# Performance work log

Measured on AMD Instinct MI355X. Metric: run time of the kernel, lower is better.

Reference implementation:

```python
import jax, jax.numpy as jnp
import numpy as np

H = 1024   # hidden_size
NH = 16    # num heads
DH = H // NH
L = 2      # attention levels
E = 8      # experts
F = 4 * H  # expert FFN hidden
B = 2
S = 1024
EPS = 1e-5
TOPK = 2
STD = 0.02


def setup_inputs() -> dict:
    key = jax.random.key(0)
    ks = jax.random.split(key, 12)
    def n(k, shp):
        return jax.random.normal(k, shp, jnp.float32) * STD
    return {
        "hidden_states": jax.random.normal(ks[0], (B, S, H), jnp.float32),
        "attention_mask": jnp.ones((B, S), jnp.int32),
        "ln1_g": jnp.ones((H,), jnp.float32), "ln1_b": jnp.zeros((H,), jnp.float32),
        "ln2_g": jnp.ones((H,), jnp.float32), "ln2_b": jnp.zeros((H,), jnp.float32),
        "Wq": n(ks[1], (L, H, H)), "Wk": n(ks[2], (L, H, H)),
        "Wv": n(ks[3], (L, H, H)), "Wo": n(ks[4], (L, H, H)),
        "bq": jnp.zeros((L, H), jnp.float32), "bk": jnp.zeros((L, H), jnp.float32),
        "bv": jnp.zeros((L, H), jnp.float32), "bo": jnp.zeros((L, H), jnp.float32),
        "level_logits": n(ks[5], (L,)),
        "Wr": n(ks[6], (H, E)), "br": jnp.zeros((E,), jnp.float32),
        "W1": n(ks[7], (E, H, F)), "b1": jnp.zeros((E, F), jnp.float32),
        "W2": n(ks[8], (E, F, H)), "b2": jnp.zeros((E, H), jnp.float32),
    }


def _ln(x, g, b):
    m = x.mean(-1, keepdims=True)
    v = x.var(-1, keepdims=True)
    return (x - m) * jax.lax.rsqrt(v + EPS) * g + b


def _mla(x, mask_f, Wq, Wk, Wv, Wo, bq, bk, bv, bo, level_logits):
    # Multi-level attention: one MHA per level, softmax-combined over levels.
    b_, s_, _ = x.shape
    def proj(W, bias):
        y = jnp.einsum('bsh,lhd->lbsd', x, W) + bias[:, None, None, :]
        return y.reshape(L, b_, s_, NH, DH)
    q, k, v = proj(Wq, bq), proj(Wk, bk), proj(Wv, bv)
    scores = jnp.einsum('lbqnd,lbknd->lbnqk', q, k) / np.float32(np.sqrt(DH))
    bias = (1.0 - mask_f)[None, :, None, None, :] * jnp.float32(-1e9)  # key-side mask
    attn = jax.nn.softmax(scores + bias, axis=-1)
    ctx = jnp.einsum('lbnqk,lbknd->lbqnd', attn, v).reshape(L, b_, s_, H)
    out = jnp.einsum('lbsh,lhd->lbsd', ctx, Wo) + bo[:, None, None, :]
    w = jax.nn.softmax(level_logits)
    return jnp.einsum('l,lbsd->bsd', w, out)


def _moe(x, Wr, br, W1, b1, W2, b2):
    # Top-2 softmax router with renormalized gates; dense expert compute,
    # sparse combine (math-equivalent to dispatch/combine without dropping).
    logits = x @ Wr + br                                  # [B,S,E]
    probs = jax.nn.softmax(logits, axis=-1)
    topv, topi = jax.lax.top_k(probs, TOPK)               # [B,S,K]
    gates = topv / topv.sum(-1, keepdims=True)
    combine = jnp.sum(jax.nn.one_hot(topi, E, dtype=x.dtype) * gates[..., None], axis=-2)  # [B,S,E]
    h = jax.nn.gelu(jnp.einsum('bsh,ehf->besf', x, W1) + b1[None, :, None, :])
    y = jnp.einsum('besf,efh->besh', h, W2) + b2[None, :, None, :]
    return jnp.einsum('bse,besh->bsh', combine, y), logits


def reference(hidden_states, attention_mask, ln1_g, ln1_b, ln2_g, ln2_b,
              Wq, Wk, Wv, Wo, bq, bk, bv, bo, level_logits,
              Wr, br, W1, b1, W2, b2):
    mask_f = attention_mask.astype(jnp.float32)
    attn = _mla(_ln(hidden_states, ln1_g, ln1_b), mask_f,
                Wq, Wk, Wv, Wo, bq, bk, bv, bo, level_logits)
    x = hidden_states + attn                  # residual 1 (dropout in eval = identity)
    moe_out, _router_logits = _moe(_ln(x, ln2_g, ln2_b), Wr, br, W1, b1, W2, b2)
    return x + moe_out                        # residual 2
```

## Files before the change

### kernel.cpp

```cpp
#include <hip/hip_runtime.h>
#include <hip/hip_bf16.h>
#include <stdint.h>

#define Hn   1024
#define NHn  16
#define DHn  64
#define Ln   2
#define En   8
#define Fn   4096
#define Bn   2
#define Sn   1024
#define Tn   2048
#define An   4096
#define KSPLIT 4

typedef __bf16 bf16_t;
typedef __bf16 bf16x2 __attribute__((ext_vector_type(2)));
typedef __bf16 bf16x4 __attribute__((ext_vector_type(4)));
typedef __bf16 bf16x8 __attribute__((ext_vector_type(8)));
typedef float  f32x4  __attribute__((ext_vector_type(4)));

__device__ __forceinline__ f32x4 mfma16(bf16x8 a, bf16x8 b, f32x4 c){
  return __builtin_amdgcn_mfma_f32_16x16x32_bf16(a, b, c, 0, 0, 0);
}
__device__ __forceinline__ void gload16(const void* gsrc, void* ldst){
  __builtin_amdgcn_global_load_lds((const __attribute__((address_space(1))) void*)gsrc,
                                   (__attribute__((address_space(3))) void*)ldst, 16, 0, 0);
}
__device__ __forceinline__ float gelu_f(float x){
  float u = 0.7978845608028654f * (x + 0.044715f * x * x * x);
  return 0.5f * x * (1.0f + tanhf(u));
}

__global__ __launch_bounds__(256)
void tcvt_k(const float* __restrict__ src, bf16_t* __restrict__ dst, int R, int C){
  __shared__ float tile[64][68];
  size_t moff = (size_t)blockIdx.z * R * C;
  src += moff; dst += moff;
  int c0 = blockIdx.x * 64, r0 = blockIdx.y * 64;
  int tid = threadIdx.x;
  int tx = tid & 15, ty = tid >> 4;
  #pragma unroll
  for (int i = 0; i < 4; ++i){
    float4 v = *(const float4*)(src + (size_t)(r0 + ty + i*16) * C + c0 + tx*4);
    *(float4*)&tile[ty + i*16][tx*4] = v;
  }
  __syncthreads();
  int c = tid >> 2, rq = tid & 3;
  #pragma unroll
  for (int i = 0; i < 2; ++i){
    int rr = (rq + i*4) * 8;
    bf16x8 pk;
    #pragma unroll
    for (int j = 0; j < 8; ++j) pk[j] = (bf16_t)tile[rr + j][c];
    *(bf16x8*)(dst + (size_t)(c0 + c) * R + r0 + rr) = pk;
  }
}

__global__ __launch_bounds__(256)
void ln_k(const float* __restrict__ x, const float* __restrict__ gam,
          const float* __restrict__ bet, bf16_t* __restrict__ out){
  int row = blockIdx.x;
  const float4* xr = (const float4*)(x + (size_t)row * Hn);
  int t = threadIdx.x, lane = t & 63, w = t >> 6;
  float4 v = xr[t];
  float s  = v.x + v.y + v.z + v.w;
  float ss = v.x*v.x + v.y*v.y + v.z*v.z + v.w*v.w;
  #pragma unroll
  for (int mk = 1; mk < 64; mk <<= 1){ s += __shfl_xor(s, mk); ss += __shfl_xor(ss, mk); }
  __shared__ float r1[4], r2[4];
  if (lane == 0){ r1[w] = s; r2[w] = ss; }
  __syncthreads();
  float S1 = r1[0]+r1[1]+r1[2]+r1[3];
  float S2 = r2[0]+r2[1]+r2[2]+r2[3];
  float mean = S1 * (1.0f/Hn);
  float var  = S2 * (1.0f/Hn) - mean*mean;
  float rstd = rsqrtf(var + 1e-5f);
  int c = t * 4;
  bf16_t* o = out + (size_t)row * Hn + c;
  o[0] = (bf16_t)((v.x-mean)*rstd*gam[c+0] + bet[c+0]);
  o[1] = (bf16_t)((v.y-mean)*rstd*gam[c+1] + bet[c+1]);
  o[2] = (bf16_t)((v.z-mean)*rstd*gam[c+2] + bet[c+2]);
  o[3] = (bf16_t)((v.w-mean)*rstd*gam[c+3] + bet[c+3]);
}

__global__ __launch_bounds__(256)
void res_ln2_k(const float* __restrict__ x, const float* __restrict__ o0,
               const float* __restrict__ o1, const float* __restrict__ lvl,
               const float* __restrict__ gam, const float* __restrict__ bet,
               float* __restrict__ x2, bf16_t* __restrict__ xn2){
  int row = blockIdx.x, t = threadIdx.x, lane = t & 63, w = t >> 6;
  float l0 = lvl[0], l1 = lvl[1];
  float mx = fmaxf(l0, l1);
  float e0 = __expf(l0 - mx), e1 = __expf(l1 - mx);
  float inv = 1.f / (e0 + e1);
  float w0 = e0 * inv, w1 = e1 * inv;
  size_t base = (size_t)row * Hn;
  float4 xv = ((const float4*)(x  + base))[t];
  float4 a0 = ((const float4*)(o0 + base))[t];
  float4 a1 = ((const float4*)(o1 + base))[t];
  float4 v;
  v.x = xv.x + w0*a0.x + w1*a1.x;
  v.y = xv.y + w0*a0.y + w1*a1.y;
  v.z = xv.z + w0*a0.z + w1*a1.z;
  v.w = xv.w + w0*a0.w + w1*a1.w;
  ((float4*)(x2 + base))[t] = v;
  float s  = v.x + v.y + v.z + v.w;
  float ss = v.x*v.x + v.y*v.y + v.z*v.z + v.w*v.w;
  #pragma unroll
  for (int mk = 1; mk < 64; mk <<= 1){ s += __shfl_xor(s, mk); ss += __shfl_xor(ss, mk); }
  __shared__ float r1[4], r2[4];
  if (lane == 0){ r1[w] = s; r2[w] = ss; }
  __syncthreads();
  float S1 = r1[0]+r1[1]+r1[2]+r1[3];
  float S2 = r2[0]+r2[1]+r2[2]+r2[3];
  float mean = S1 * (1.0f/Hn);
  float var  = S2 * (1.0f/Hn) - mean*mean;
  float rstd = rsqrtf(var + 1e-5f);
  int c = t * 4;
  bf16_t* o = xn2 + base + c;
  o[0] = (bf16_t)((v.x-mean)*rstd*gam[c+0] + bet[c+0]);
  o[1] = (bf16_t)((v.y-mean)*rstd*gam[c+1] + bet[c+1]);
  o[2] = (bf16_t)((v.z-mean)*rstd*gam[c+2] + bet[c+2]);
  o[3] = (bf16_t)((v.w-mean)*rstd*gam[c+3] + bet[c+3]);
}

struct GP {
  const bf16_t* A;
  const bf16_t* Bt;
  const float*  bias;
  float*        fout;
  bf16_t*       bfout;
  const int*    list;
  const int*    counts;
  int Kstride;
  int Kloc;
};

template<int MODE>
__global__ __launch_bounds__(256)
void gemm_k(GP p){
  constexpr int BM  = 128;
  constexpr int ACH = BM / 64;
  constexpr int WRT = BM / 2;
  constexpr int Mf  = WRT / 16;
  const int nt = blockIdx.x, mt = blockIdx.y, z = blockIdx.z;
  const bf16_t* A = p.A;
  const bf16_t* Bt = p.Bt;
  const float* bias = p.bias;
  const int* list = nullptr;
  int cnt = 0x7fffffff;
  int kbase = 0;
  if constexpr (MODE == 0){
    Bt += (size_t)z*Hn*Hn; bias += z*Hn;
  } else if constexpr (MODE == 1){
    Bt += (size_t)z*Hn*Hn; bias += z*Hn; A += (size_t)z*Bn*Sn*Hn;
  } else if constexpr (MODE == 3){
    cnt = p.counts[z];
    if (mt * BM >= cnt) return;
    list = p.list + z * Tn;
    Bt += (size_t)z*Fn*Hn; bias += z*Fn;
  } else {
    int e = z >> 2;
    cnt = p.counts[e];
    if (mt * BM >= cnt) return;
    list = p.list + e * Tn;
    Bt += (size_t)e*Hn*Fn; bias += e*Hn;
    kbase = (z & 3) * (Fn / KSPLIT);
  }
  const int Ks = p.Kstride;
  const int NT = p.Kloc >> 5;

  __shared__ bf16_t As[2][BM*32];
  __shared__ bf16_t Bs[2][128*32];
  const int tid = threadIdx.x, lane = tid & 63, w = tid >> 6;
  const int wr = (w >> 1) * WRT, wc = (w & 1) * 64;
  const int lane15 = lane & 15, kg = lane >> 4;

  const bf16_t* aptr[ACH];
  int achk[ACH];
  #pragma unroll
  for (int i = 0; i < ACH; ++i){
    int ch = tid + i*256;
    achk[i] = ch;
    int row = ch >> 2, kc = (ch & 3) * 8;
    int ar;
    if constexpr (MODE == 3){ int g = mt*BM + row; if (g >= cnt) g = cnt - 1; ar = list[g] >> 1; }
    else if constexpr (MODE == 4){ int g = mt*BM + row; if (g >= cnt) g = cnt - 1; ar = list[g]; }
    else ar = mt*BM + row;
    aptr[i] = A + (size_t)ar * Ks + kbase + kc;
  }
  const bf16_t* bptr[2];
  int bchk[2];
  #pragma unroll
  for (int i = 0; i < 2; ++i){
    int ch = tid + i*256;
    bchk[i] = ch;
    int row = ch >> 2, kc = (ch & 3) * 8;
    bptr[i] = Bt + (size_t)(nt*128 + row) * Ks + kbase + kc;
  }

  const f32x4 fz = {0.f,0.f,0.f,0.f};
  f32x4 acc[Mf][4];
  #pragma unroll
  for (int m = 0; m < Mf; ++m)
    #pragma unroll
    for (int n = 0; n < 4; ++n) acc[m][n] = fz;

  #pragma unroll
  for (int i = 0; i < ACH; ++i) gload16(aptr[i], &As[0][achk[i]*8]);
  #pragma unroll
  for (int i = 0; i < 2; ++i)   gload16(bptr[i], &Bs[0][bchk[i]*8]);
  __syncthreads();

  int cur = 0;
  for (int t = 0; t < NT; ++t){
    if (t + 1 < NT){
      int k1 = (t+1) * 32;
      #pragma unroll
      for (int i = 0; i < ACH; ++i) gload16(aptr[i] + k1, &As[cur^1][achk[i]*8]);
      #pragma unroll
      for (int i = 0; i < 2; ++i)   gload16(bptr[i] + k1, &Bs[cur^1][bchk[i]*8]);
    }
    bf16x8 af[Mf], bfr[4];
    #pragma unroll
    for (int m = 0; m < Mf; ++m) af[m]  = *(const bf16x8*)(&As[cur][(wr + m*16 + lane15)*32 + kg*8]);
    #pragma unroll
    for (int n = 0; n < 4; ++n)  bfr[n] = *(const bf16x8*)(&Bs[cur][(wc + n*16 + lane15)*32 + kg*8]);
    #pragma unroll
    for (int m = 0; m < Mf; ++m)
      #pragma unroll
      for (int n = 0; n < 4; ++n)
        acc[m][n] = mfma16(af[m], bfr[n], acc[m][n]);
    __syncthreads();
    cur ^= 1;
  }

  if constexpr (MODE == 0){
    bf16_t* outp = p.bfout + (size_t)z * (Bn*NHn*Sn*DHn);
    if (z < 4){
      #pragma unroll
      for (int m = 0; m < Mf; ++m){
        int row0 = mt*BM + wr + m*16 + kg*4;
        #pragma unroll
        for (int n = 0; n < 4; ++n){
          int col = nt*128 + wc + n*16 + lane15;
          int nh = col >> 6, dh = col & 63;
          float bv = bias[col];
          f32x4 v = acc[m][n];
          #pragma unroll
          for (int r = 0; r < 4; ++r){
            int tk = row0 + r;
            int bb = tk >> 10, s = tk & 1023;
            outp[((size_t)(bb*NHn + nh)*Sn + s)*DHn + dh] = (bf16_t)(v[r] + bv);
          }
        }
      }
    } else {
      #pragma unroll
      for (int m = 0; m < Mf; ++m){
        int row0 = mt*BM + wr + m*16 + kg*4;
        int bb = row0 >> 10, s = row0 & 1023;
        #pragma unroll
        for (int n = 0; n < 4; ++n){
          int col = nt*128 + wc + n*16 + lane15;
          int nh = col >> 6, dh = col & 63;
          float bv = bias[col];
          f32x4 v = acc[m][n];
          bf16x4 pk;
          pk[0] = (bf16_t)(v[0] + bv);
          pk[1] = (bf16_t)(v[1] + bv);
          pk[2] = (bf16_t)(v[2] + bv);
          pk[3] = (bf16_t)(v[3] + bv);
          *(bf16x4*)(outp + ((size_t)(bb*NHn + nh)*DHn + dh)*Sn + s) = pk;
        }
      }
    }
  } else if constexpr (MODE == 1){
    float* outp = p.fout + (size_t)z * Tn * Hn;
    #pragma unroll
    for (int m = 0; m < Mf; ++m){
      int row0 = mt*BM + wr + m*16 + kg*4;
      #pragma unroll
      for (int n = 0; n < 4; ++n){
        int col = nt*128 + wc + n*16 + lane15;
        float bv = bias[col];
        f32x4 v = acc[m][n];
        #pragma unroll
        for (int r = 0; r < 4; ++r)
          outp[(size_t)(row0 + r)*Hn + col] = v[r] + bv;
      }
    }
  } else if constexpr (MODE == 3){
    #pragma unroll
    for (int m = 0; m < Mf; ++m){
      int row0 = mt*BM + wr + m*16 + kg*4;
      #pragma unroll
      for (int n = 0; n < 4; ++n){
        int col = nt*128 + wc + n*16 + lane15;
        float bv = bias[col];
        f32x4 v = acc[m][n];
        #pragma unroll
        for (int r = 0; r < 4; ++r){
          int g = row0 + r;
          if (g < cnt){
            int aid = list[g];
            p.bfout[(size_t)aid*Fn + col] = (bf16_t)gelu_f(v[r] + bv);
          }
        }
      }
    }
  } else {
    bf16_t* outp = p.bfout + (size_t)(z & 3) * An * Hn;
    bool addb = (z & 3) == 0;
    #pragma unroll
    for (int m = 0; m < Mf; ++m){
      int row0 = mt*BM + wr + m*16 + kg*4;
      #pragma unroll
      for (int n = 0; n < 4; ++n){
        int col = nt*128 + wc + n*16 + lane15;
        float bv = addb ? bias[col] : 0.f;
        f32x4 v = acc[m][n];
        #pragma unroll
        for (int r = 0; r < 4; ++r){
          int g = row0 + r;
          if (g < cnt){
            int aid = list[g];
            outp[(size_t)aid*Hn + col] = (bf16_t)(v[r] + bv);
          }
        }
      }
    }
  }
}

__global__ __launch_bounds__(256)
void attn_k(const bf16_t* __restrict__ qh, const bf16_t* __restrict__ kh,
            const bf16_t* __restrict__ vtb, const int* __restrict__ amask,
            bf16_t* __restrict__ ctxb){
  int z  = blockIdx.x;
  int qb = blockIdx.y;
  int lvl = z >> 5, bb = (z >> 4) & 1, nh = z & 15;
  int tid = threadIdx.x, lane = tid & 63, w = tid >> 6;
  int lane15 = lane & 15, kg = lane >> 4;
  const bf16_t* Q  = qh  + (size_t)z * Sn * DHn;
  const bf16_t* Kp = kh  + (size_t)z * Sn * DHn;
  const bf16_t* Vt = vtb + (size_t)z * DHn * Sn;
  const int* mrow = amask + bb * Sn;
  __shared__ bf16_t Ks[2][32*64];
  __shared__ bf16_t Vs[2][64*32];
  __shared__ float bias_lds[Sn];
  __shared__ bf16_t p_lds[4][16*40];
  {
    int4 mv = ((const int4*)mrow)[tid];
    float4 bv;
    bv.x = mv.x ? 0.f : -1e9f;
    bv.y = mv.y ? 0.f : -1e9f;
    bv.z = mv.z ? 0.f : -1e9f;
    bv.w = mv.w ? 0.f : -1e9f;
    ((float4*)bias_lds)[tid] = bv;
  }
  int krow = w*8 + (lane >> 3);
  const bf16_t* ksrc = Kp + (size_t)krow*DHn + (((lane&7) ^ (krow&7)) << 3);
  int vrow = w*16 + (lane >> 2);
  const bf16_t* vsrc = Vt + (size_t)vrow*Sn + ((((lane&3) ^ ((vrow>>2)&3))) << 3);
  bf16_t* kdst[2] = { &Ks[0][w*512 + lane*8], &Ks[1][w*512 + lane*8] };
  bf16_t* vdst[2] = { &Vs[0][w*512 + lane*8], &Vs[1][w*512 + lane*8] };

  const f32x4 fz = {0.f,0.f,0.f,0.f};
  int qt = qb*4 + w;
  int qr = qt*16 + lane15;
  bf16x8 qa0 = *(const bf16x8*)(Q + (size_t)qr*DHn + kg*8);
  bf16x8 qa1 = *(const bf16x8*)(Q + (size_t)qr*DHn + 32 + kg*8);
  f32x4 ctxa[4] = {fz, fz, fz, fz};
  float m_ln = -1e30f;
  float s_ln = 0.f;
  float m_out[4] = {-1e30f,-1e30f,-1e30f,-1e30f};

  const int kslot0 = (kg ^ (lane15 & 7));
  const int kslot1 = ((kg + 4) ^ (lane15 & 7));
  const int ka_off0 = lane15*64 + kslot0*8;
  const int ka_off1 = lane15*64 + kslot1*8;
  const int kb_off0 = (16 + lane15)*64 + kslot0*8;
  const int kb_off1 = (16 + lane15)*64 + kslot1*8;

  gload16(ksrc, kdst[0]);
  gload16(vsrc, vdst[0]);
  __syncthreads();

  for (int kc = 0; kc < 32; ++kc){
    const int cur = kc & 1;
    const bf16_t* Kb = Ks[cur];
    const bf16_t* Vb = Vs[cur];
    if (kc + 1 < 32){
      gload16(ksrc + (size_t)(kc+1)*32*DHn, kdst[cur^1]);
      gload16(vsrc + (kc+1)*32,             vdst[cur^1]);
    }
    int k0 = kc * 32;
    bf16x8 ka0 = *(const bf16x8*)(Kb + ka_off0);
    bf16x8 ka1 = *(const bf16x8*)(Kb + ka_off1);
    bf16x8 kb0 = *(const bf16x8*)(Kb + kb_off0);
    bf16x8 kb1 = *(const bf16x8*)(Kb + kb_off1);
    f32x4 sA = mfma16(ka1, qa1, mfma16(ka0, qa0, fz));
    f32x4 sB = mfma16(kb1, qa1, mfma16(kb0, qa0, fz));
    float4 biasA = *(const float4*)(bias_lds + k0 + kg*4);
    float4 biasB = *(const float4*)(bias_lds + k0 + 16 + kg*4);
    float sv[8];
    sv[0] = sA[0]*0.125f + biasA.x;
    sv[1] = sA[1]*0.125f + biasA.y;
    sv[2] = sA[2]*0.125f + biasA.z;
    sv[3] = sA[3]*0.125f + biasA.w;
    sv[4] = sB[0]*0.125f + biasB.x;
    sv[5] = sB[1]*0.125f + biasB.y;
    sv[6] = sB[2]*0.125f + biasB.z;
    sv[7] = sB[3]*0.125f + biasB.w;
    float mx = fmaxf(fmaxf(fmaxf(sv[0],sv[1]),fmaxf(sv[2],sv[3])),
                     fmaxf(fmaxf(sv[4],sv[5]),fmaxf(sv[6],sv[7])));
    mx = fmaxf(mx, __shfl_xor(mx, 16));
    mx = fmaxf(mx, __shfl_xor(mx, 32));
    if (!__all(mx <= m_ln)){
      float mnew = fmaxf(m_ln, mx);
      s_ln *= __expf(m_ln - mnew);
      #pragma unroll
      for (int r = 0; r < 4; ++r){
        float mo = __shfl(mnew, kg*4 + r);
        float corr = __expf(m_out[r] - mo);
        ctxa[0][r] *= corr; ctxa[1][r] *= corr; ctxa[2][r] *= corr; ctxa[3][r] *= corr;
        m_out[r] = mo;
      }
      m_ln = mnew;
    }
    float pv[8];
    #pragma unroll
    for (int j = 0; j < 8; ++j){ pv[j] = __expf(sv[j] - m_ln); s_ln += pv[j]; }
    bf16_t* pr = p_lds[w] + lane15*40;
    *(bf16x2*)(pr + kg*4)          = (bf16x2){(bf16_t)pv[0], (bf16_t)pv[1]};
    *(bf16x2*)(pr + kg*4 + 2)      = (bf16x2){(bf16_t)pv[2], (bf16_t)pv[3]};
    *(bf16x2*)(pr + 16 + kg*4)     = (bf16x2){(bf16_t)pv[4], (bf16_t)pv[5]};
    *(bf16x2*)(pr + 16 + kg*4 + 2) = (bf16x2){(bf16_t)pv[6], (bf16_t)pv[7]};
    bf16x8 paf = *(const bf16x8*)(p_lds[w] + lane15*40 + kg*8);
    #pragma unroll
    for (int df = 0; df < 4; ++df){
      int r = df*16 + lane15;
      bf16x8 vbf = *(const bf16x8*)(Vb + r*32 + ((kg ^ ((r>>2)&3)) << 3));
      ctxa[df] = mfma16(paf, vbf, ctxa[df]);
    }
    __syncthreads();
  }
  s_ln += __shfl_xor(s_ln, 16);
  s_ln += __shfl_xor(s_ln, 32);
  #pragma unroll
  for (int r = 0; r < 4; ++r){
    float inv = 1.f / __shfl(s_ln, kg*4 + r);
    int srow = qt*16 + kg*4 + r;
    #pragma unroll
    for (int df = 0; df < 4; ++df){
      int d = df*16 + lane15;
      ctxb[((size_t)(lvl*2 + bb)*Sn + srow)*Hn + nh*DHn + d] = (bf16_t)(ctxa[df][r] * inv);
    }
  }
}

__global__ __launch_bounds__(64)
void router_k(const float* __restrict__ x2, const float* __restrict__ gam,
              const float* __restrict__ bet, const float* __restrict__ Wr,
              const float* __restrict__ br, float* __restrict__ gates,
              int* __restrict__ lists, int* __restrict__ counts){
  int t = blockIdx.x, lane = threadIdx.x;
  const float4* xr = (const float4*)(x2 + (size_t)t * Hn);
  float4 vbuf[4];
  float s = 0.f, ss = 0.f;
  #pragma unroll
  for (int i = 0; i < 4; ++i){
    float4 v = xr[lane + i*64];
    vbuf[i] = v;
    s  += v.x + v.y + v.z + v.w;
    ss += v.x*v.x + v.y*v.y + v.z*v.z + v.w*v.w;
  }
  #pragma unroll
  for (int mk = 1; mk < 64; mk <<= 1){ s += __shfl_xor(s, mk); ss += __shfl_xor(ss, mk); }
  float mean = s * (1.0f/Hn);
  float var  = ss * (1.0f/Hn) - mean*mean;
  float rstd = rsqrtf(var + 1e-5f);
  float a[8] = {0,0,0,0,0,0,0,0};
  #pragma unroll
  for (int i = 0; i < 4; ++i){
    int c = (lane + i*64) * 4;
    float4 v = vbuf[i];
    float xn[4] = {
      (v.x-mean)*rstd*gam[c+0] + bet[c+0],
      (v.y-mean)*rstd*gam[c+1] + bet[c+1],
      (v.z-mean)*rstd*gam[c+2] + bet[c+2],
      (v.w-mean)*rstd*gam[c+3] + bet[c+3]};
    #pragma unroll
    for (int j = 0; j < 4; ++j){
      const float* w = Wr + (size_t)(c + j) * En;
      #pragma unroll
      for (int e8 = 0; e8 < 8; ++e8) a[e8] += xn[j] * w[e8];
    }
  }
  #pragma unroll
  for (int e8 = 0; e8 < 8; ++e8)
    #pragma unroll
    for (int mk = 1; mk < 64; mk <<= 1) a[e8] += __shfl_xor(a[e8], mk);
  if (lane == 0){
    float lg[8]; float mx = -1e30f;
    #pragma unroll
    for (int e8 = 0; e8 < 8; ++e8){ lg[e8] = a[e8] + br[e8]; mx = fmaxf(mx, lg[e8]); }
    float p[8];
    #pragma unroll
    for (int e8 = 0; e8 < 8; ++e8) p[e8] = __expf(lg[e8] - mx);
    int i0 = 0; float v0 = p[0];
    #pragma unroll
    for (int e8 = 1; e8 < 8; ++e8) if (p[e8] > v0){ v0 = p[e8]; i0 = e8; }
    int i1 = -1; float v1 = -1.f;
    #pragma unroll
    for (int e8 = 0; e8 < 8; ++e8) if (e8 != i0 && p[e8] > v1){ v1 = p[e8]; i1 = e8; }
    float g0 = v0 / (v0 + v1), g1 = v1 / (v0 + v1);
    gates[2*t] = g0; gates[2*t+1] = g1;
    int s0 = atomicAdd(&counts[i0], 1); lists[i0*Tn + s0] = 2*t;
    int s1 = atomicAdd(&counts[i1], 1); lists[i1*Tn + s1] = 2*t + 1;
  }
}

__global__ __launch_bounds__(256)
void comb_k(const float* __restrict__ x2, const bf16_t* __restrict__ P,
            const float* __restrict__ gates, float* __restrict__ out){
  int t = blockIdx.x, i = threadIdx.x;
  float g0 = gates[2*t], g1 = gates[2*t+1];
  const size_t PS = (size_t)An * Hn;
  f32x4 s0 = {0,0,0,0}, s1 = {0,0,0,0};
  #pragma unroll
  for (int ks = 0; ks < KSPLIT; ++ks){
    bf16x4 u0 = *(const bf16x4*)(P + ks*PS + (size_t)(2*t)*Hn + i*4);
    bf16x4 u1 = *(const bf16x4*)(P + ks*PS + (size_t)(2*t+1)*Hn + i*4);
    #pragma unroll
    for (int j = 0; j < 4; ++j){ s0[j] += (float)u0[j]; s1[j] += (float)u1[j]; }
  }
  f32x4 va = ((const f32x4*)(x2 + (size_t)t*Hn))[i];
  f32x4 o = va + g0*s0 + g1*s1;
  ((f32x4*)(out + (size_t)t*Hn))[i] = o;
}

extern "C" void kernel_launch(void* const* d_in, const int* in_sizes, int n_in,
                              void* d_out, int out_size, void* d_ws, size_t ws_size,
                              hipStream_t stream)
{
  const float* x    = (const float*)d_in[0];
  const int* amask  = (const int*)d_in[1];
  const float* ln1g = (const float*)d_in[2];
  const float* ln1b = (const float*)d_in[3];
  const float* ln2g = (const float*)d_in[4];
  const float* ln2b = (const float*)d_in[5];
  const float* Wq   = (const float*)d_in[6];
  const float* Wk   = (const float*)d_in[7];
  const float* Wv   = (const float*)d_in[8];
  const float* Wo   = (const float*)d_in[9];
  const float* bq   = (const float*)d_in[10];
  const float* bk   = (const float*)d_in[11];
  const float* bv   = (const float*)d_in[12];
  const float* bo   = (const float*)d_in[13];
  const float* lvl  = (const float*)d_in[14];
  const float* Wr   = (const float*)d_in[15];
  const float* br   = (const float*)d_in[16];
  const float* W1   = (const float*)d_in[17];
  const float* b1   = (const float*)d_in[18];
  const float* W2   = (const float*)d_in[19];
  const float* b2   = (const float*)d_in[20];
  float* out = (float*)d_out;
  (void)in_sizes; (void)n_in; (void)out_size; (void)ws_size;

  char* wsp = (char*)d_ws;
  auto nxt = [&](size_t bytes) -> char* {
    char* r = wsp; wsp += (bytes + 255) & ~(size_t)255; return r;
  };
  bf16_t* wqkvT = (bf16_t*)nxt((size_t)6*Hn*Hn*2);
  bf16_t* woT   = (bf16_t*)nxt((size_t)Ln*Hn*Hn*2);
  bf16_t* w1t   = (bf16_t*)nxt((size_t)En*Fn*Hn*2);
  bf16_t* w2t   = (bf16_t*)nxt((size_t)En*Hn*Fn*2);
  float*  bqkv  = (float*)nxt((size_t)6*Hn*4);
  bf16_t* xn1   = (bf16_t*)nxt((size_t)Tn*Hn*2);
  bf16_t* qkvh  = (bf16_t*)nxt((size_t)6*Bn*NHn*Sn*DHn*2);
  bf16_t* ctxb  = (bf16_t*)nxt((size_t)Ln*Bn*Sn*Hn*2);
  float*  otmp  = (float*)nxt((size_t)Ln*Tn*Hn*4);
  float*  x2    = (float*)nxt((size_t)Tn*Hn*4);
  bf16_t* xn2   = (bf16_t*)nxt((size_t)Tn*Hn*2);
  float*  gates = (float*)nxt((size_t)Tn*2*4);
  int*    lists = (int*)nxt((size_t)En*Tn*4);
  int*    counts= (int*)nxt(256);
  bf16_t* hbuf  = (bf16_t*)nxt((size_t)An*Fn*2);
  bf16_t* ybuf  = (bf16_t*)nxt((size_t)KSPLIT*An*Hn*2);

  hipMemsetAsync(counts, 0, En*sizeof(int), stream);
  hipMemcpyAsync(bqkv,          bq, (size_t)Ln*Hn*4, hipMemcpyDeviceToDevice, stream);
  hipMemcpyAsync(bqkv + 2*Hn,   bk, (size_t)Ln*Hn*4, hipMemcpyDeviceToDevice, stream);
  hipMemcpyAsync(bqkv + 4*Hn,   bv, (size_t)Ln*Hn*4, hipMemcpyDeviceToDevice, stream);

  tcvt_k<<<dim3(16,16,Ln), 256, 0, stream>>>(Wq, wqkvT,            Hn, Hn);
  tcvt_k<<<dim3(16,16,Ln), 256, 0, stream>>>(Wk, wqkvT + 2*Hn*Hn,  Hn, Hn);
  tcvt_k<<<dim3(16,16,Ln), 256, 0, stream>>>(Wv, wqkvT + 4*Hn*Hn,  Hn, Hn);
  tcvt_k<<<dim3(16,16,Ln), 256, 0, stream>>>(Wo, woT,              Hn, Hn);
  tcvt_k<<<dim3(Fn/64, Hn/64, En), 256, 0, stream>>>(W1, w1t, Hn, Fn);
  tcvt_k<<<dim3(Hn/64, Fn/64, En), 256, 0, stream>>>(W2, w2t, Fn, Hn);

  ln_k<<<Tn, 256, 0, stream>>>(x, ln1g, ln1b, xn1);

  { GP g{};
    g.A = xn1; g.Bt = wqkvT; g.bias = bqkv; g.bfout = qkvh;
    g.Kstride = Hn; g.Kloc = Hn;
    gemm_k<0><<<dim3(8,16,6), 256, 0, stream>>>(g); }

  {
    const bf16_t* qh = qkvh;
    const bf16_t* kh = qkvh + (size_t)2*Bn*NHn*Sn*DHn;
    const bf16_t* vt = qkvh + (size_t)4*Bn*NHn*Sn*DHn;
    attn_k<<<dim3(Ln*Bn*NHn, Sn/64), 256, 0, stream>>>(qh, kh, vt, amask, ctxb);
  }

  { GP g{};
    g.A = ctxb; g.Bt = woT; g.bias = bo; g.fout = otmp;
    g.Kstride = Hn; g.Kloc = Hn;
    gemm_k<1><<<dim3(8,16,2), 256, 0, stream>>>(g); }

  res_ln2_k<<<Tn, 256, 0, stream>>>(x, otmp, otmp + (size_t)Tn*Hn, lvl,
                                    ln2g, ln2b, x2, xn2);
  router_k<<<Tn, 64, 0, stream>>>(x2, ln2g, ln2b, Wr, br, gates, lists, counts);

  { GP g{};
    g.A = xn2; g.Bt = w1t; g.bias = b1; g.bfout = hbuf;
    g.list = lists; g.counts = counts;
    g.Kstride = Hn; g.Kloc = Hn;
    gemm_k<3><<<dim3(Fn/128, Tn/128, En), 256, 0, stream>>>(g); }
  { GP g{};
    g.A = hbuf; g.Bt = w2t; g.bfout = ybuf; g.bias = b2;
    g.list = lists; g.counts = counts;
    g.Kstride = Fn; g.Kloc = Fn / KSPLIT;
    gemm_k<4><<<dim3(Hn/128, Tn/128, En*KSPLIT), 256, 0, stream>>>(g); }

  comb_k<<<Tn, 256, 0, stream>>>(x2, ybuf, gates, out);
}
```

Measured before the change: 499.3 us.

## Replace early-exit MoE GEMM grids with persistent compact-scheduled expert kernels

```diff
diff --git a/kernel.cpp b/kernel.cpp
--- a/kernel.cpp
+++ b/kernel.cpp
@@ -140,77 +140,46 @@
 template<int MODE>
 __global__ __launch_bounds__(256)
 void gemm_k(GP p){
-  constexpr int BM  = 128;
-  constexpr int ACH = BM / 64;
-  constexpr int WRT = BM / 2;
-  constexpr int Mf  = WRT / 16;
   const int nt = blockIdx.x, mt = blockIdx.y, z = blockIdx.z;
   const bf16_t* A = p.A;
   const bf16_t* Bt = p.Bt;
   const float* bias = p.bias;
-  const int* list = nullptr;
-  int cnt = 0x7fffffff;
-  int kbase = 0;
   if constexpr (MODE == 0){
     Bt += (size_t)z*Hn*Hn; bias += z*Hn;
-  } else if constexpr (MODE == 1){
+  } else {
     Bt += (size_t)z*Hn*Hn; bias += z*Hn; A += (size_t)z*Bn*Sn*Hn;
-  } else if constexpr (MODE == 3){
-    cnt = p.counts[z];
-    if (mt * BM >= cnt) return;
-    list = p.list + z * Tn;
-    Bt += (size_t)z*Fn*Hn; bias += z*Fn;
-  } else {
-    int e = z >> 2;
-    cnt = p.counts[e];
-    if (mt * BM >= cnt) return;
-    list = p.list + e * Tn;
-    Bt += (size_t)e*Hn*Fn; bias += e*Hn;
-    kbase = (z & 3) * (Fn / KSPLIT);
   }
   const int Ks = p.Kstride;
   const int NT = p.Kloc >> 5;
 
-  __shared__ bf16_t As[2][BM*32];
+  __shared__ bf16_t As[2][128*32];
   __shared__ bf16_t Bs[2][128*32];
   const int tid = threadIdx.x, lane = tid & 63, w = tid >> 6;
-  const int wr = (w >> 1) * WRT, wc = (w & 1) * 64;
+  const int wr = (w >> 1) * 64, wc = (w & 1) * 64;
   const int lane15 = lane & 15, kg = lane >> 4;
 
-  const bf16_t* aptr[ACH];
-  int achk[ACH];
-  #pragma unroll
-  for (int i = 0; i < ACH; ++i){
-    int ch = tid + i*256;
-    achk[i] = ch;
-    int row = ch >> 2, kc = (ch & 3) * 8;
-    int ar;
-    if constexpr (MODE == 3){ int g = mt*BM + row; if (g >= cnt) g = cnt - 1; ar = list[g] >> 1; }
-    else if constexpr (MODE == 4){ int g = mt*BM + row; if (g >= cnt) g = cnt - 1; ar = list[g]; }
-    else ar = mt*BM + row;
-    aptr[i] = A + (size_t)ar * Ks + kbase + kc;
-  }
+  const bf16_t* aptr[2];
   const bf16_t* bptr[2];
-  int bchk[2];
   #pragma unroll
   for (int i = 0; i < 2; ++i){
     int ch = tid + i*256;
-    bchk[i] = ch;
     int row = ch >> 2, kc = (ch & 3) * 8;
-    bptr[i] = Bt + (size_t)(nt*128 + row) * Ks + kbase + kc;
+    aptr[i] = A  + (size_t)(mt*128 + row) * Ks + kc;
+    bptr[i] = Bt + (size_t)(nt*128 + row) * Ks + kc;
   }
 
   const f32x4 fz = {0.f,0.f,0.f,0.f};
-  f32x4 acc[Mf][4];
-  #pragma unroll
-  for (int m = 0; m < Mf; ++m)
+  f32x4 acc[4][4];
+  #pragma unroll
+  for (int m = 0; m < 4; ++m)
     #pragma unroll
     for (int n = 0; n < 4; ++n) acc[m][n] = fz;
 
   #pragma unroll
-  for (int i = 0; i < ACH; ++i) gload16(aptr[i], &As[0][achk[i]*8]);
-  #pragma unroll
-  for (int i = 0; i < 2; ++i)   gload16(bptr[i], &Bs[0][bchk[i]*8]);
+  for (int i = 0; i < 2; ++i){
+    gload16(aptr[i], &As[0][(tid + i*256)*8]);
+    gload16(bptr[i], &Bs[0][(tid + i*256)*8]);
+  }
   __syncthreads();
 
   int cur = 0;
@@ -218,17 +187,18 @@
     if (t + 1 < NT){
       int k1 = (t+1) * 32;
       #pragma unroll
-      for (int i = 0; i < ACH; ++i) gload16(aptr[i] + k1, &As[cur^1][achk[i]*8]);
-      #pragma unroll
-      for (int i = 0; i < 2; ++i)   gload16(bptr[i] + k1, &Bs[cur^1][bchk[i]*8]);
-    }
-    bf16x8 af[Mf], bfr[4];
-    #pragma unroll
-    for (int m = 0; m < Mf; ++m) af[m]  = *(const bf16x8*)(&As[cur][(wr + m*16 + lane15)*32 + kg*8]);
+      for (int i = 0; i < 2; ++i){
+        gload16(aptr[i] + k1, &As[cur^1][(tid + i*256)*8]);
+        gload16(bptr[i] + k1, &Bs[cur^1][(tid + i*256)*8]);
+      }
+    }
+    bf16x8 af[4], bfr[4];
+    #pragma unroll
+    for (int m = 0; m < 4; ++m) af[m]  = *(const bf16x8*)(&As[cur][(wr + m*16 + lane15)*32 + kg*8]);
     #pragma unroll
     for (int n = 0; n < 4; ++n)  bfr[n] = *(const bf16x8*)(&Bs[cur][(wc + n*16 + lane15)*32 + kg*8]);
     #pragma unroll
-    for (int m = 0; m < Mf; ++m)
+    for (int m = 0; m < 4; ++m)
       #pragma unroll
       for (int n = 0; n < 4; ++n)
         acc[m][n] = mfma16(af[m], bfr[n], acc[m][n]);
@@ -240,8 +210,8 @@
     bf16_t* outp = p.bfout + (size_t)z * (Bn*NHn*Sn*DHn);
     if (z < 4){
       #pragma unroll
-      for (int m = 0; m < Mf; ++m){
-        int row0 = mt*BM + wr + m*16 + kg*4;
+      for (int m = 0; m < 4; ++m){
+        int row0 = mt*128 + wr + m*16 + kg*4;
         #pragma unroll
         for (int n = 0; n < 4; ++n){
           int col = nt*128 + wc + n*16 + lane15;
@@ -258,8 +228,8 @@
       }
     } else {
       #pragma unroll
-      for (int m = 0; m < Mf; ++m){
-        int row0 = mt*BM + wr + m*16 + kg*4;
+      for (int m = 0; m < 4; ++m){
+        int row0 = mt*128 + wr + m*16 + kg*4;
         int bb = row0 >> 10, s = row0 & 1023;
         #pragma unroll
         for (int n = 0; n < 4; ++n){
@@ -276,11 +246,11 @@
         }
       }
     }
-  } else if constexpr (MODE == 1){
+  } else {
     float* outp = p.fout + (size_t)z * Tn * Hn;
     #pragma unroll
-    for (int m = 0; m < Mf; ++m){
-      int row0 = mt*BM + wr + m*16 + kg*4;
+    for (int m = 0; m < 4; ++m){
+      int row0 = mt*128 + wr + m*16 + kg*4;
       #pragma unroll
       for (int n = 0; n < 4; ++n){
         int col = nt*128 + wc + n*16 + lane15;
@@ -291,42 +261,143 @@
           outp[(size_t)(row0 + r)*Hn + col] = v[r] + bv;
       }
     }
-  } else if constexpr (MODE == 3){
-    #pragma unroll
-    for (int m = 0; m < Mf; ++m){
-      int row0 = mt*BM + wr + m*16 + kg*4;
-      #pragma unroll
-      for (int n = 0; n < 4; ++n){
-        int col = nt*128 + wc + n*16 + lane15;
-        float bv = bias[col];
-        f32x4 v = acc[m][n];
+  }
+}
+
+template<int MODE>
+__global__ __launch_bounds__(256)
+void moe_k(GP p){
+  constexpr int NGRP = (MODE == 3) ? 2 : 4;
+  constexpr int NTW  = (MODE == 3) ? 16 : 8;
+  const int bid = blockIdx.x;
+  const int x = bid & 7;
+  const int tid = threadIdx.x, lane = tid & 63, w = tid >> 6;
+  const int lane15 = lane & 15, kg = lane >> 4;
+  const int wr = (w >> 1) * 64, wc = (w & 1) * 64;
+  __shared__ bf16_t As[2][128*32];
+  __shared__ bf16_t Bs[2][128*32];
+  const f32x4 fz = {0.f,0.f,0.f,0.f};
+
+  int colTotal = 0;
+  #pragma unroll
+  for (int m2 = 0; m2 < NGRP; ++m2){
+    int gq = x + m2*8;
+    int eq = (MODE == 3) ? (gq >> 1) : (gq >> 2);
+    colTotal += ((p.counts[eq] + 127) >> 7) * NTW;
+  }
+
+  for (int j = bid >> 3; j < colTotal; j += 160){
+    int rem = j, g = -1;
+    #pragma unroll
+    for (int m2 = 0; m2 < NGRP; ++m2){
+      int gq = x + m2*8;
+      int eq = (MODE == 3) ? (gq >> 1) : (gq >> 2);
+      int ng = ((p.counts[eq] + 127) >> 7) * NTW;
+      if (g < 0){ if (rem < ng) g = gq; else rem -= ng; }
+    }
+    int e, ks, mt, nt;
+    if constexpr (MODE == 3){
+      e = g >> 1; ks = 0;
+      mt = rem >> 4; nt = ((g & 1) << 4) | (rem & 15);
+    } else {
+      e = g >> 2; ks = g & 3;
+      mt = rem >> 3; nt = rem & 7;
+    }
+    const int cnt = p.counts[e];
+    const int* list = p.list + e * Tn;
+    int off = 0;
+    #pragma unroll
+    for (int q = 0; q < En; ++q){ if (q < e) off += p.counts[q]; }
+
+    const int Ks    = (MODE == 3) ? Hn : Fn;
+    const int kbase = (MODE == 3) ? 0 : ks * (Fn / KSPLIT);
+    const bf16_t* Bt = p.Bt + (size_t)e * Fn * Hn;
+    const float* bias = p.bias + ((MODE == 3) ? e*Fn : e*Hn);
+
+    const bf16_t* aptr[2];
+    const bf16_t* bptr[2];
+    #pragma unroll
+    for (int i = 0; i < 2; ++i){
+      int ch = tid + i*256;
+      int row = ch >> 2, kc = (ch & 3) * 8;
+      int gi = mt*128 + row; if (gi >= cnt) gi = cnt - 1;
+      int ar = (MODE == 3) ? (list[gi] >> 1) : (off + gi);
+      aptr[i] = p.A + (size_t)ar * Ks + kbase + kc;
+      bptr[i] = Bt + (size_t)(nt*128 + row) * Ks + kbase + kc;
+    }
+
+    f32x4 acc[4][4];
+    #pragma unroll
+    for (int m = 0; m < 4; ++m)
+      #pragma unroll
+      for (int n = 0; n < 4; ++n) acc[m][n] = fz;
+
+    #pragma unroll
+    for (int i = 0; i < 2; ++i){
+      gload16(aptr[i], &As[0][(tid + i*256)*8]);
+      gload16(bptr[i], &Bs[0][(tid + i*256)*8]);
+    }
+    __syncthreads();
+
+    int cur = 0;
+    for (int t = 0; t < 32; ++t){
+      if (t + 1 < 32){
+        int k1 = (t+1) * 32;
         #pragma unroll
-        for (int r = 0; r < 4; ++r){
-          int g = row0 + r;
-          if (g < cnt){
-            int aid = list[g];
-            p.bfout[(size_t)aid*Fn + col] = (bf16_t)gelu_f(v[r] + bv);
+        for (int i = 0; i < 2; ++i){
+          gload16(aptr[i] + k1, &As[cur^1][(tid + i*256)*8]);
+          gload16(bptr[i] + k1, &Bs[cur^1][(tid + i*256)*8]);
+        }
+      }
+      bf16x8 af[4], bfr[4];
+      #pragma unroll
+      for (int m = 0; m < 4; ++m) af[m]  = *(const bf16x8*)(&As[cur][(wr + m*16 + lane15)*32 + kg*8]);
+      #pragma unroll
+      for (int n = 0; n < 4; ++n)  bfr[n] = *(const bf16x8*)(&Bs[cur][(wc + n*16 + lane15)*32 + kg*8]);
+      #pragma unroll
+      for (int m = 0; m < 4; ++m)
+        #pragma unroll
+        for (int n = 0; n < 4; ++n)
+          acc[m][n] = mfma16(af[m], bfr[n], acc[m][n]);
+      __syncthreads();
+      cur ^= 1;
+    }
+
+    if constexpr (MODE == 3){
+      #pragma unroll
+      for (int m = 0; m < 4; ++m){
+        int row0 = mt*128 + wr + m*16 + kg*4;
+        #pragma unroll
+        for (int n = 0; n < 4; ++n){
+          int col = nt*128 + wc + n*16 + lane15;
+          float bv = bias[col];
+          f32x4 v = acc[m][n];
+          #pragma unroll
+          for (int r = 0; r < 4; ++r){
+            int gi = row0 + r;
+            if (gi < cnt)
+              p.bfout[(size_t)(off + gi)*Fn + col] = (bf16_t)gelu_f(v[r] + bv);
           }
         }
       }
-    }
-  } else {
-    bf16_t* outp = p.bfout + (size_t)(z & 3) * An * Hn;
-    bool addb = (z & 3) == 0;
-    #pragma unroll
-    for (int m = 0; m < Mf; ++m){
-      int row0 = mt*BM + wr + m*16 + kg*4;
-      #pragma unroll
-      for (int n = 0; n < 4; ++n){
-        int col = nt*128 + wc + n*16 + lane15;
-        float bv = addb ? bias[col] : 0.f;
-        f32x4 v = acc[m][n];
+    } else {
+      bf16_t* outp = p.bfout + (size_t)ks * An * Hn;
+      bool addb = (ks == 0);
+      #pragma unroll
+      for (int m = 0; m < 4; ++m){
+        int row0 = mt*128 + wr + m*16 + kg*4;
         #pragma unroll
-        for (int r = 0; r < 4; ++r){
-          int g = row0 + r;
-          if (g < cnt){
-            int aid = list[g];
-            outp[(size_t)aid*Hn + col] = (bf16_t)(v[r] + bv);
+        for (int n = 0; n < 4; ++n){
+          int col = nt*128 + wc + n*16 + lane15;
+          float bv = addb ? bias[col] : 0.f;
+          f32x4 v = acc[m][n];
+          #pragma unroll
+          for (int r = 0; r < 4; ++r){
+            int gi = row0 + r;
+            if (gi < cnt){
+              int aid = list[gi];
+              outp[(size_t)aid*Hn + col] = (bf16_t)(v[r] + bv);
+            }
           }
         }
       }
@@ -629,13 +700,11 @@
   { GP g{};
     g.A = xn2; g.Bt = w1t; g.bias = b1; g.bfout = hbuf;
     g.list = lists; g.counts = counts;
-    g.Kstride = Hn; g.Kloc = Hn;
-    gemm_k<3><<<dim3(Fn/128, Tn/128, En), 256, 0, stream>>>(g); }
+    moe_k<3><<<dim3(1280,1,1), 256, 0, stream>>>(g); }
   { GP g{};
     g.A = hbuf; g.Bt = w2t; g.bfout = ybuf; g.bias = b2;
     g.list = lists; g.counts = counts;
-    g.Kstride = Fn; g.Kloc = Fn / KSPLIT;
-    gemm_k<4><<<dim3(Hn/128, Tn/128, En*KSPLIT), 256, 0, stream>>>(g); }
+    moe_k<4><<<dim3(1280,1,1), 256, 0, stream>>>(g); }
 
   comb_k<<<Tn, 256, 0, stream>>>(x2, ybuf, gates, out);
 }
```

Result: slower. 520.0 us (+4.2%).
